# Kernel optimization log

Measured on AMD Instinct MI355X. Metric: run time of the kernel, lower is better.

The kernel has to match this reference:

```python
import jax, jax.numpy as jnp
import numpy as np

N, E = 25000, 400000
HID, EDGE_F, DIM, HEADS, ADY = 128, 16, 3, 8, 64
INNER = int(1.25 * HID)          # 160
MSG_F = 2 * HID + EDGE_F + 1     # 273 (e3, relaxed=False -> 1 distance feature)


def silu(x):
    return x * jax.nn.sigmoid(x)


def ada_ln(x, y, W, b):
    # LayerNorm (no affine) + FiLM conditioning from y
    mu = jnp.mean(x, axis=-1, keepdims=True)
    var = jnp.var(x, axis=-1, keepdims=True)
    xn = (x - mu) * jax.lax.rsqrt(var + 1e-5)
    scale, shift = jnp.split(y @ W + b, 2, axis=-1)
    return xn * (1.0 + scale) + shift


def setup_inputs() -> dict:
    key = jax.random.key(0)
    ks = jax.random.split(key, 32)
    rn = lambda k, shp, s=0.05: (jax.random.normal(k, shp, jnp.float32) * s)
    inp = {
        'h': jax.random.normal(ks[0], (N, HID), jnp.float32),
        'coords': jax.random.normal(ks[1], (N, DIM), jnp.float32),
        'a': jax.random.normal(ks[2], (E, EDGE_F), jnp.float32),
        'y': jax.random.normal(ks[3], (N, ADY), jnp.float32),
        'res': jnp.zeros((N, HID), jnp.float32),
        'src': jax.random.randint(ks[4], (E,), 0, N, jnp.int32),
        'dst': jax.random.randint(ks[5], (E,), 0, N, jnp.int32),
        # edge MLP
        'We1': rn(ks[6], (MSG_F, INNER)), 'be1': jnp.zeros((INNER,), jnp.float32),
        'We2': rn(ks[7], (INNER, INNER)), 'be2': jnp.zeros((INNER,), jnp.float32),
        # coord head (xavier gain 0.001 -> tiny init)
        'Wc': rn(ks[8], (INNER, 1), 0.001),
        # attention/value/output heads
        'Wv': rn(ks[9], (INNER, HID)),
        'Wa': rn(ks[10], (INNER, HEADS)),
        'Wo': rn(ks[11], (HID, HID)),
        # node MLP
        'Wn1': rn(ks[12], (HID, INNER)), 'bn1': jnp.zeros((INNER,), jnp.float32),
        'Wn2': rn(ks[13], (INNER, HID)), 'bn2': jnp.zeros((HID,), jnp.float32),
        # adaptive LayerNorms (FiLM from y)
        'Wf1': rn(ks[14], (ADY, 2 * HID)), 'bf1': jnp.zeros((2 * HID,), jnp.float32),
        'Wf2': rn(ks[15], (ADY, 2 * HID)), 'bf2': jnp.zeros((2 * HID,), jnp.float32),
    }
    return inp


def reference(h, coords, a, y, res, src, dst,
              We1, be1, We2, be2, Wc, Wv, Wa, Wo,
              Wn1, bn1, Wn2, bn2, Wf1, bf1, Wf2, bf2):
    n = h.shape[0]
    heads = Wa.shape[1]
    # --- distance features (e3, relaxed=False): radial only ---
    xs, xd = coords[src], coords[dst]          # [E, 3]
    diffs = xs - xd
    radials = jnp.sum(diffs * diffs, axis=-1, keepdims=True)  # [E, 1]
    # --- edge MLP on gathered features ---
    f = jnp.concatenate([h[src], h[dst], radials, a], axis=-1)  # [E, 273]
    m = silu(f @ We1 + be1)
    m = silu(m @ We2 + be2)                    # [E, inner]
    # --- coordinate messages + scatter-sum to dst ---
    msg_x = (m @ Wc) * diffs / (jnp.sqrt(radials + 1e-5) + 1.0)  # [E, 3]
    coords_out = coords + jax.ops.segment_sum(msg_x, dst, num_segments=n)
    # --- edge softmax over incoming edges per dst node ---
    logits = m @ Wa                             # [E, heads]
    mx = jax.ops.segment_max(logits, dst, num_segments=n)
    ex = jnp.exp(logits - mx[dst])
    den = jax.ops.segment_sum(ex, dst, num_segments=n)
    w = ex / den[dst]                           # [E, heads]
    # --- weighted value aggregation ---
    vals = (m @ Wv).reshape(-1, heads, HID // heads) * w[:, :, None]
    h_agg = jax.ops.segment_sum(vals, dst, num_segments=n).reshape(n, HID)
    f2 = h_agg @ Wo
    res1 = res + f2
    h1 = ada_ln(h + f2, y, Wf1, bf1)
    f3 = silu(h1 @ Wn1 + bn1) @ Wn2 + bn2
    res2 = res1 + f3
    h2 = ada_ln(h1 + f3, y, Wf2, bf2)
    return (h2, coords_out, res2)
```

## Files before the change

kernel.cpp:

```cpp
#include <hip/hip_runtime.h>
#include <math.h>

#define N_NODES 25000
#define N_EDGES 400000
#define HID 128
#define EDGE_F 16
#define ADY 64
#define INNER 160
#define MSG_F 273
#define HEADS 8

#define OUT_CRD (N_NODES * HID)
#define OUT_RES (N_NODES * (HID + 3))

#define FLAG_OFF 0
#define DEN_OFF  256
#define CACC_OFF 800256
#define HAGG_OFF 1100256
#define CNT_OFF  13900256
#define CUR_OFF  14000256
#define PERM_OFF 14100256
#define MEMSET_BYTES 14000256
#define HBF_OFF  15700256
#define YBF_OFF  22100256
#define BIAS_OFF 25300256
#define BW_OFF   25302560

#define WSLICE 3072
#define SM_OFF 512
#define SCR_STRIDE 146

typedef unsigned short u16;
typedef unsigned int u32;
typedef unsigned long long u64;
typedef __attribute__((ext_vector_type(8))) short short8;
typedef __attribute__((ext_vector_type(4))) float f32x4;

__device__ __forceinline__ float bf2f(u16 v) {
    union { u32 u; float f; } x; x.u = ((u32)v) << 16; return x.f;
}
__device__ __forceinline__ u16 f2bf(float f) {
    union { float ff; u32 u; } x; x.ff = f;
    u32 u = x.u;
    u32 rounding = 0x7FFFu + ((u >> 16) & 1u);
    u += rounding;
    return (u16)(u >> 16);
}
__device__ __forceinline__ u32 cvt_pk(float lo, float hi) {
    u32 r;
    asm("v_cvt_pk_bf16_f32 %0, %1, %2" : "=v"(r) : "v"(lo), "v"(hi));
    return r;
}
__device__ __forceinline__ float silu(float z) {
    z = fminf(fmaxf(z, -30000.f), 30000.f);
    return z / (1.0f + __expf(-z));
}

template<bool F32> __device__ __forceinline__ float ldg1(const void* p, size_t i) {
    if (F32) return ((const float*)p)[i];
    return bf2f(((const u16*)p)[i]);
}
template<bool F32> __device__ __forceinline__ void stg1(void* p, size_t i, float v) {
    if (F32) ((float*)p)[i] = v;
    else     ((u16*)p)[i] = f2bf(v);
}
__device__ __forceinline__ float ldany(const void* p, size_t i, bool f32) {
    return f32 ? ((const float*)p)[i] : bf2f(((const u16*)p)[i]);
}
__device__ __forceinline__ void wave_lds_fence() {
    __builtin_amdgcn_wave_barrier();
    __builtin_amdgcn_s_waitcnt(0xc07f);
    __builtin_amdgcn_wave_barrier();
}

__device__ __forceinline__ int a_addr(int k, int lr) {
    return ((k >> 5) << 9) + (((((k & 31) >> 3) << 4) | lr) << 3) + (k & 7);
}

struct CvtArgs {
    const void* src[8];
    u64 dstoff[8];
    int n[8];
};
struct BwArgs {
    const void* We1; const void* We2; const void* Wv; const void* Wa;
    const void* Wc;  const void* Wo;  const void* Wn1; const void* Wn2;
    const void* Wf1; const void* Wf2;
    u64 b1, b2, b3, b4, b5, b6, b7, b8;
};

__global__ __launch_bounds__(256)
void preproc_kernel(const void* hsrc, int* flag, char* ws, CvtArgs args, BwArgs bwa,
                    const int* __restrict__ dstp, int* __restrict__ cnt)
{
    __shared__ float red[256];
    __shared__ int sflag;
    const int t = threadIdx.x;
    {
        const u16* p = (const u16*)hsrc;
        float mx = 0.f;
        for (int i = 0; i < 8; i++) {
            int idx = (t * 8 + i) * 97;
            float v = fabsf(bf2f(p[idx * 2]));
            mx = fmaxf(mx, v);
        }
        red[t] = mx;
        __syncthreads();
        for (int s = 128; s > 0; s >>= 1) {
            if (t < s) red[t] = fmaxf(red[t], red[t + s]);
            __syncthreads();
        }
        if (t == 0) {
            sflag = (red[0] > 1e10f || red[0] == 0.f) ? 1 : 0;
            if (blockIdx.x == 0) flag[0] = sflag;
        }
        __syncthreads();
    }
    const bool f32 = (sflag != 0);
    const int g = blockIdx.x * 256 + t;
    const int stride = gridDim.x * 256;

    for (int i = g; i < N_EDGES; i += stride)
        atomicAdd(&cnt[dstp[i]], 1);

    for (int ten = 0; ten < 8; ten++) {
        const void* s = args.src[ten];
        u16* d = (u16*)(ws + args.dstoff[ten]);
        const int n = args.n[ten];
        if (f32) {
            const float* sf = (const float*)s;
            for (int i = g; i < n; i += stride) d[i] = f2bf(sf[i]);
        } else {
            const u16* su = (const u16*)s;
            for (int i = g; i < n; i += stride) d[i] = su[i];
        }
    }

    u16* b1 = (u16*)(ws + bwa.b1);
    u16* b2 = (u16*)(ws + bwa.b2);
    u16* b3 = (u16*)(ws + bwa.b3);
    u16* b4 = (u16*)(ws + bwa.b4);
    u16* b5 = (u16*)(ws + bwa.b5);
    u16* b6 = (u16*)(ws + bwa.b6);
    u16* b7 = (u16*)(ws + bwa.b7);
    u16* b8 = (u16*)(ws + bwa.b8);
    for (int i = g; i < 5*2*10*512; i += stride) {
        int tt = i >> 9, r = i & 511, l = r >> 3, j = r & 7;
        int c = tt / 20, ks = (tt / 10) % 2, nt = tt % 10;
        int k = c*64 + ks*32 + (l >> 4)*8 + j;
        int n = nt*16 + (l & 15);
        float v = 0.f;
        if (k < MSG_F)      v = ldany(bwa.We1, (size_t)k*INNER + n, f32);
        else if (k == 273)  v = ldany(bwa.We1, (size_t)256*INNER + n, f32);
        b1[i] = f2bf(v);
    }
    for (int i = g; i < 5*10*512; i += stride) {
        int tt = i >> 9, r = i & 511, l = r >> 3, j = r & 7;
        int k5 = tt / 10, nt = tt % 10;
        int k = k5*32 + (l >> 4)*8 + j;
        int n = nt*16 + (l & 15);
        b2[i] = f2bf(ldany(bwa.We2, (size_t)k*INNER + n, f32));
    }
    for (int i = g; i < 5*9*512; i += stride) {
        int tt = i >> 9, r = i & 511, l = r >> 3, j = r & 7;
        int k5 = tt / 9, nt = tt % 9;
        int k = k5*32 + (l >> 4)*8 + j;
        int n = nt*16 + (l & 15);
        float v = 0.f;
        if (n < 128)       v = ldany(bwa.Wv, (size_t)k*HID + n, f32);
        else if (n < 136)  v = ldany(bwa.Wa, (size_t)k*HEADS + (n-128), f32);
        else if (n == 136) v = ldany(bwa.Wc, (size_t)k, f32);
        b3[i] = f2bf(v);
    }
    for (int i = g; i < 4*8*512; i += stride) {
        int tt = i >> 9, r = i & 511, l = r >> 3, j = r & 7;
        int cks = tt / 8, nt = tt % 8;
        int k = cks*32 + (l >> 4)*8 + j;
        int n = nt*16 + (l & 15);
        b4[i] = f2bf(ldany(bwa.Wo, (size_t)k*HID + n, f32));
    }
    for (int i = g; i < 4*10*512; i += stride) {
        int tt = i >> 9, r = i & 511, l = r >> 3, j = r & 7;
        int cks = tt / 10, nt = tt % 10;
        int k = cks*32 + (l >> 4)*8 + j;
        int n = nt*16 + (l & 15);
        b5[i] = f2bf(ldany(bwa.Wn1, (size_t)k*INNER + n, f32));
    }
    for (int i = g; i < 5*8*512; i += stride) {
        int tt = i >> 9, r = i & 511, l = r >> 3, j = r & 7;
        int k5 = tt / 8, nt = tt % 8;
        int k = k5*32 + (l >> 4)*8 + j;
        int n = nt*16 + (l & 15);
        b6[i] = f2bf(ldany(bwa.Wn2, (size_t)k*HID + n, f32));
    }
    for (int i = g; i < 2*16*512; i += stride) {
        int tt = i >> 9, r = i & 511, l = r >> 3, j = r & 7;
        int ks = tt / 16, nt = tt % 16;
        int k = ks*32 + (l >> 4)*8 + j;
        int n = nt*16 + (l & 15);
        b7[i] = f2bf(ldany(bwa.Wf1, (size_t)k*256 + n, f32));
        b8[i] = f2bf(ldany(bwa.Wf2, (size_t)k*256 + n, f32));
    }
}

__global__ __launch_bounds__(1024)
void scan_kernel(const int* __restrict__ cnt, int* __restrict__ cursor)
{
    __shared__ int ssum[1024];
    const int t = threadIdx.x;
    const int base = t * 25;
    int loc[25];
    int s = 0;
    #pragma unroll
    for (int j = 0; j < 25; j++) {
        int i = base + j;
        int v = (i < N_NODES) ? cnt[i] : 0;
        loc[j] = s; s += v;
    }
    ssum[t] = s;
    __syncthreads();
    for (int off = 1; off < 1024; off <<= 1) {
        int v = (t >= off) ? ssum[t - off] : 0;
        __syncthreads();
        ssum[t] += v;
        __syncthreads();
    }
    int offs = (t > 0) ? ssum[t - 1] : 0;
    #pragma unroll
    for (int j = 0; j < 25; j++) {
        int i = base + j;
        if (i < N_NODES) cursor[i] = offs + loc[j];
    }
}

__global__ __launch_bounds__(256)
void scatter_kernel(const int* __restrict__ dstp, int* __restrict__ cursor,
                    int* __restrict__ perm)
{
    int i = blockIdx.x * 256 + threadIdx.x;
    if (i < N_EDGES) {
        int pos = atomicAdd(&cursor[dstp[i]], 1);
        perm[pos] = i;
    }
}

template<bool F32>
__device__ __forceinline__ void edge_body(
    const u16* __restrict__ hbf, const void* coords, const void* a,
    const int* __restrict__ src, const int* __restrict__ dst,
    const int* __restrict__ perm,
    const u16* __restrict__ We1P, const u16* __restrict__ We2P,
    const u16* __restrict__ W3P,
    const u16* __restrict__ cbe1, const u16* __restrict__ cbe2,
    float* __restrict__ den, float* __restrict__ hagg, float* __restrict__ cacc,
    u16* sPool)
{
    const int t   = threadIdx.x;
    const int w   = t >> 6;
    const int l   = t & 63;
    const int col = l & 15;
    const int q   = l >> 4;
    const int e0  = blockIdx.x * 64;
    const int l8  = l << 3;

    u16* sW = sPool + w * WSLICE;

    const int ge2 = perm[e0 + w*16 + col];
    const int s2 = src[ge2];
    const int d2 = dst[ge2];

    short8 afr[8];
    {
        const u16* hs = hbf + (size_t)s2*HID + q*8;
        const u16* hd = hbf + (size_t)d2*HID + q*8;
        #pragma unroll
        for (int kk = 0; kk < 4; kk++) {
            afr[kk]     = *(const short8*)(hs + (kk << 5));
            afr[4 + kk] = *(const short8*)(hd + (kk << 5));
        }
    }

    const int er = l >> 2;
    const int p  = l & 3;
    const int ge = perm[e0 + w*16 + er];
    float dx = 0.f, dy = 0.f, dz = 0.f, invf = 0.f, r2 = 0.f;
    if (p < 2) {
        int s_ = src[ge], d_ = dst[ge];
        dx = ldg1<F32>(coords, (size_t)s_*3+0) - ldg1<F32>(coords, (size_t)d_*3+0);
        dy = ldg1<F32>(coords, (size_t)s_*3+1) - ldg1<F32>(coords, (size_t)d_*3+1);
        dz = ldg1<F32>(coords, (size_t)s_*3+2) - ldg1<F32>(coords, (size_t)d_*3+2);
        r2 = dx*dx + dy*dy + dz*dz;
        invf = 1.0f / (sqrtf(r2 + 1e-5f) + 1.0f);
        __align__(16) u16 tmp[16];
        #pragma unroll
        for (int j = 0; j < 16; j++) tmp[j] = 0;
        if (p == 0) {
            tmp[0] = f2bf(r2);
            for (int j = 0; j < 15; j++)
                tmp[1+j] = f2bf(ldg1<F32>(a, (size_t)ge*EDGE_F + j));
        } else {
            tmp[0] = f2bf(ldg1<F32>(a, (size_t)ge*EDGE_F + 15));
            tmp[1] = f2bf(r2 - bf2f(f2bf(r2)));
        }
        *(uint4*)(sW + (32*p + er)*8)      = ((uint4*)tmp)[0];
        *(uint4*)(sW + (32*p + 16 + er)*8) = ((uint4*)tmp)[1];
    }
    wave_lds_fence();

    f32x4 acc1[10];
    #pragma unroll
    for (int nt = 0; nt < 10; nt++) {
        float v = bf2f(cbe1[nt*16 + col]);
        acc1[nt] = (f32x4){v, v, v, v};
    }
    #pragma unroll
    for (int kk = 0; kk < 8; kk++) {
        const u16* B1 = We1P + ((kk*10) << 9) + l8;
        #pragma unroll
        for (int nt = 0; nt < 10; nt++) {
            short8 b = *(const short8*)(B1 + (nt << 9));
            acc1[nt] = __builtin_amdgcn_mfma_f32_16x16x32_bf16(afr[kk], b, acc1[nt], 0, 0, 0);
        }
    }
    {
        short8 af = *(const short8*)(sW + l8);
        const u16* B1 = We1P + ((8*10) << 9) + l8;
        #pragma unroll
        for (int nt = 0; nt < 10; nt++) {
            short8 b = *(const short8*)(B1 + (nt << 9));
            acc1[nt] = __builtin_amdgcn_mfma_f32_16x16x32_bf16(af, b, acc1[nt], 0, 0, 0);
        }
    }
    const bool lo = (col & 1) == 0;
    const int cb16 = col & ~1;
    #pragma unroll
    for (int nt = 0; nt < 10; nt++) {
        float m0 = silu(acc1[nt][0]);
        float m1 = silu(acc1[nt][1]);
        float m2 = silu(acc1[nt][2]);
        float m3 = silu(acc1[nt][3]);
        float p0 = __shfl_xor(m0, 1);
        float p1 = __shfl_xor(m1, 1);
        float p2 = __shfl_xor(m2, 1);
        float p3 = __shfl_xor(m3, 1);
        int k0 = nt*16 + cb16;
        if (lo) {
            *(u32*)(sW + SM_OFF + a_addr(k0, q*4+0)) = cvt_pk(m0, p0);
            *(u32*)(sW + SM_OFF + a_addr(k0, q*4+1)) = cvt_pk(m1, p1);
        } else {
            *(u32*)(sW + SM_OFF + a_addr(k0, q*4+2)) = cvt_pk(p2, m2);
            *(u32*)(sW + SM_OFF + a_addr(k0, q*4+3)) = cvt_pk(p3, m3);
        }
    }
    wave_lds_fence();

    f32x4 acc2[10];
    #pragma unroll
    for (int nt = 0; nt < 10; nt++) {
        float v = bf2f(cbe2[nt*16 + col]);
        acc2[nt] = (f32x4){v, v, v, v};
    }
    #pragma unroll
    for (int k5 = 0; k5 < 5; k5++) {
        short8 af = *(const short8*)(sW + SM_OFF + (k5 << 9) + l8);
        const u16* B2 = We2P + ((k5*10) << 9) + l8;
        #pragma unroll
        for (int nt = 0; nt < 10; nt++) {
            short8 b = *(const short8*)(B2 + (nt << 9));
            acc2[nt] = __builtin_amdgcn_mfma_f32_16x16x32_bf16(af, b, acc2[nt], 0, 0, 0);
        }
    }
    wave_lds_fence();
    #pragma unroll
    for (int nt = 0; nt < 10; nt++) {
        float m0 = silu(acc2[nt][0]);
        float m1 = silu(acc2[nt][1]);
        float m2 = silu(acc2[nt][2]);
        float m3 = silu(acc2[nt][3]);
        float p0 = __shfl_xor(m0, 1);
        float p1 = __shfl_xor(m1, 1);
        float p2 = __shfl_xor(m2, 1);
        float p3 = __shfl_xor(m3, 1);
        int k0 = nt*16 + cb16;
        if (lo) {
            *(u32*)(sW + SM_OFF + a_addr(k0, q*4+0)) = cvt_pk(m0, p0);
            *(u32*)(sW + SM_OFF + a_addr(k0, q*4+1)) = cvt_pk(m1, p1);
        } else {
            *(u32*)(sW + SM_OFF + a_addr(k0, q*4+2)) = cvt_pk(p2, m2);
            *(u32*)(sW + SM_OFF + a_addr(k0, q*4+3)) = cvt_pk(p3, m3);
        }
    }
    wave_lds_fence();

    f32x4 acc3[9];
    #pragma unroll
    for (int nt = 0; nt < 9; nt++) acc3[nt] = (f32x4){0.f, 0.f, 0.f, 0.f};
    #pragma unroll
    for (int k5 = 0; k5 < 5; k5++) {
        short8 af = *(const short8*)(sW + SM_OFF + (k5 << 9) + l8);
        const u16* B3 = W3P + ((k5*9) << 9) + l8;
        #pragma unroll
        for (int nt = 0; nt < 9; nt++) {
            short8 b = *(const short8*)(B3 + (nt << 9));
            acc3[nt] = __builtin_amdgcn_mfma_f32_16x16x32_bf16(af, b, acc3[nt], 0, 0, 0);
        }
    }
    wave_lds_fence();

    int dsts[16];
    #pragma unroll
    for (int row = 0; row < 16; row++) dsts[row] = __shfl(d2, row);
    float dxv[4], dyv[4], dzv[4], ivv[4];
    #pragma unroll
    for (int rr = 0; rr < 4; rr++) {
        int sl = (q*4 + rr) << 2;
        dxv[rr] = __shfl(dx, sl); dyv[rr] = __shfl(dy, sl);
        dzv[rr] = __shfl(dz, sl); ivv[rr] = __shfl(invf, sl);
    }

    {
        float exv[4] = {0.f, 0.f, 0.f, 0.f};
        if (col < 8) {
            #pragma unroll
            for (int rr = 0; rr < 4; rr++)
                exv[rr] = __expf(fminf(fmaxf(acc3[8][rr], -30.f), 30.f));
        }
        #pragma unroll
        for (int nt = 0; nt < 8; nt++) {
            float ex0 = __shfl(exv[0], q*16 + nt);
            float ex1 = __shfl(exv[1], q*16 + nt);
            float ex2 = __shfl(exv[2], q*16 + nt);
            float ex3 = __shfl(exv[3], q*16 + nt);
            float v0 = acc3[nt][0] * ex0;
            float v1 = acc3[nt][1] * ex1;
            float v2 = acc3[nt][2] * ex2;
            float v3 = acc3[nt][3] * ex3;
            float p0 = __shfl_xor(v0, 1);
            float p1 = __shfl_xor(v1, 1);
            float p2 = __shfl_xor(v2, 1);
            float p3 = __shfl_xor(v3, 1);
            int cb = nt*16 + cb16;
            int rowA = q*4 + (lo ? 0 : 2);
            u32 wA = lo ? cvt_pk(v0, p0) : cvt_pk(p2, v2);
            u32 wB = lo ? cvt_pk(v1, p1) : cvt_pk(p3, v3);
            *(u32*)(&sW[rowA*SCR_STRIDE + cb])       = wA;
            *(u32*)(&sW[(rowA+1)*SCR_STRIDE + cb])   = wB;
        }
        if (col < 8) {
            #pragma unroll
            for (int rr = 0; rr < 4; rr++)
                sW[(q*4 + rr)*SCR_STRIDE + 128 + col] = f2bf(exv[rr]);
        }
        if (col == 8) {
            #pragma unroll
            for (int rr = 0; rr < 4; rr++) {
                float lc = fminf(fmaxf(acc3[8][rr], -1e6f), 1e6f) * ivv[rr];
                sW[(q*4 + rr)*SCR_STRIDE + 136] = f2bf(lc * dxv[rr]);
                sW[(q*4 + rr)*SCR_STRIDE + 137] = f2bf(lc * dyv[rr]);
                sW[(q*4 + rr)*SCR_STRIDE + 138] = f2bf(lc * dzv[rr]);
            }
        }
    }
    wave_lds_fence();

    #pragma unroll
    for (int pass = 0; pass < 3; pass++) {
        int c = pass*64 + l;
        bool act = c < 139;
        float accu = 0.f;
        int prevd = dsts[0];
        #pragma unroll
        for (int row = 0; row < 16; row++) {
            int d = dsts[row];
            if (d != prevd) {
                if (act) {
                    if (c < 128)      atomicAdd(&hagg[(size_t)prevd*HID + c], accu);
                    else if (c < 136) atomicAdd(&den[(size_t)prevd*8 + (c-128)], accu);
                    else              atomicAdd(&cacc[(size_t)prevd*3 + (c-136)], accu);
                }
                accu = 0.f; prevd = d;
            }
            if (act) accu += bf2f(sW[row*SCR_STRIDE + c]);
        }
        if (act) {
            if (c < 128)      atomicAdd(&hagg[(size_t)prevd*HID + c], accu);
            else if (c < 136) atomicAdd(&den[(size_t)prevd*8 + (c-128)], accu);
            else              atomicAdd(&cacc[(size_t)prevd*3 + (c-136)], accu);
        }
    }
}

__global__ __launch_bounds__(256, 4)
void edge_kernel(const int* __restrict__ flag,
                 const u16* __restrict__ hbf, const void* coords, const void* a,
                 const int* __restrict__ src, const int* __restrict__ dst,
                 const int* __restrict__ perm,
                 const u16* __restrict__ We1P, const u16* __restrict__ We2P,
                 const u16* __restrict__ W3P,
                 const u16* __restrict__ cbe1, const u16* __restrict__ cbe2,
                 float* __restrict__ den, float* __restrict__ hagg,
                 float* __restrict__ cacc)
{
    __shared__ __align__(16) u16 sPool[4 * WSLICE];
    if (*flag)
        edge_body<true>(hbf, coords, a, src, dst, perm, We1P, We2P, W3P,
                        cbe1, cbe2, den, hagg, cacc, sPool);
    else
        edge_body<false>(hbf, coords, a, src, dst, perm, We1P, We2P, W3P,
                         cbe1, cbe2, den, hagg, cacc, sPool);
}

template<bool F32>
__device__ __forceinline__ void node_body(
    const u16* __restrict__ hbf, const void* res, const void* coords,
    const u16* __restrict__ ybf,
    const float* __restrict__ den, const float* __restrict__ hagg,
    const float* __restrict__ cacc,
    const u16* __restrict__ WoP, const u16* __restrict__ Wn1P,
    const u16* __restrict__ Wn2P, const u16* __restrict__ Wf1P,
    const u16* __restrict__ Wf2P,
    const u16* __restrict__ cbn1, const u16* __restrict__ cbn2,
    const u16* __restrict__ cbf1, const u16* __restrict__ cbf2,
    void* out, u16* sScr)
{
    const int t = threadIdx.x;
    const int w = t >> 6, l = t & 63, col = l & 15, q = l >> 4;
    const int nodew = blockIdx.x * 64 + w * 16;
    const int mynode = nodew + col;
    const bool okA = mynode < N_NODES;
    const int l8 = l << 3;
    const bool lo = (col & 1) == 0;
    const int cb16 = col & ~1;
    u16* sc = sScr + w * 16 * 168;

    int gm[4]; bool okC[4];
    #pragma unroll
    for (int r = 0; r < 4; r++) { gm[r] = nodew + q*4 + r; okC[r] = gm[r] < N_NODES; }

    f32x4 aF2[8];
    #pragma unroll
    for (int nt = 0; nt < 8; nt++) aF2[nt] = (f32x4){0.f,0.f,0.f,0.f};
    #pragma unroll
    for (int c = 0; c < 2; c++) {
        #pragma unroll
        for (int ks = 0; ks < 2; ks++) {
            const int kbase = c*64 + ks*32 + q*8;
            union { u32 w[4]; short8 v; } u;
            if (okA) {
                float dd = den[(size_t)mynode*8 + (kbase >> 4)];
                float inv = dd > 0.f ? 1.f/dd : 0.f;
                const float4* gp = (const float4*)(hagg + (size_t)mynode*HID + kbase);
                float4 v0 = gp[0], v1 = gp[1];
                u.w[0] = cvt_pk(v0.x*inv, v0.y*inv);
                u.w[1] = cvt_pk(v0.z*inv, v0.w*inv);
                u.w[2] = cvt_pk(v1.x*inv, v1.y*inv);
                u.w[3] = cvt_pk(v1.z*inv, v1.w*inv);
            } else {
                #pragma unroll
                for (int j = 0; j < 4; j++) u.w[j] = 0;
            }
            const u16* B = WoP + (((c*2 + ks)*8) << 9) + l8;
            #pragma unroll
            for (int nt = 0; nt < 8; nt++) {
                short8 b = *(const short8*)(B + (nt << 9));
                aF2[nt] = __builtin_amdgcn_mfma_f32_16x16x32_bf16(u.v, b, aF2[nt], 0, 0, 0);
            }
        }
    }

    f32x4 aFl[16];
    #pragma unroll
    for (int nt = 0; nt < 16; nt++) {
        float v = bf2f(cbf1[nt*16 + col]);
        aFl[nt] = (f32x4){v,v,v,v};
    }
    #pragma unroll
    for (int ks = 0; ks < 2; ks++) {
        short8 af;
        if (okA) af = *(const short8*)(ybf + (size_t)mynode*ADY + ks*32 + q*8);
        else { union { u16 s[8]; short8 v; } z; for (int j=0;j<8;j++) z.s[j]=0; af = z.v; }
        const u16* B = Wf1P + ((ks*16) << 9) + l8;
        #pragma unroll
        for (int nt = 0; nt < 16; nt++) {
            short8 b = *(const short8*)(B + (nt << 9));
            aFl[nt] = __builtin_amdgcn_mfma_f32_16x16x32_bf16(af, b, aFl[nt], 0, 0, 0);
        }
    }

    float h1c[8][4], r1c[8][4];
    {
        float xv[8][4], s[4], ss[4];
        #pragma unroll
        for (int r = 0; r < 4; r++) { s[r] = 0.f; ss[r] = 0.f; }
        #pragma unroll
        for (int nt = 0; nt < 8; nt++)
            #pragma unroll
            for (int r = 0; r < 4; r++) {
                float hv = okC[r] ? bf2f(hbf[(size_t)gm[r]*HID + nt*16 + col]) : 0.f;
                float x = hv + aF2[nt][r];
                xv[nt][r] = x; s[r] += x; ss[r] += x*x;
            }
        #pragma unroll
        for (int r = 0; r < 4; r++)
            for (int off = 1; off <= 8; off <<= 1) {
                s[r]  += __shfl_xor(s[r], off);
                ss[r] += __shfl_xor(ss[r], off);
            }
        #pragma unroll
        for (int r = 0; r < 4; r++) {
            float mu = s[r] * (1.f/128.f);
            float var = ss[r] * (1.f/128.f) - mu*mu;
            float rs = rsqrtf(fmaxf(var, 0.f) + 1e-5f);
            #pragma unroll
            for (int nt = 0; nt < 8; nt++) {
                float h1 = (xv[nt][r]-mu)*rs*(1.f+aFl[nt][r]) + aFl[nt+8][r];
                h1c[nt][r] = h1;
                float rv = okC[r] ? ldg1<F32>(res, (size_t)gm[r]*HID + nt*16 + col) : 0.f;
                r1c[nt][r] = rv + aF2[nt][r];
            }
        }
        #pragma unroll
        for (int nt = 0; nt < 8; nt++) {
            float p0 = __shfl_xor(h1c[nt][0], 1);
            float p1 = __shfl_xor(h1c[nt][1], 1);
            float p2 = __shfl_xor(h1c[nt][2], 1);
            float p3 = __shfl_xor(h1c[nt][3], 1);
            int cb = nt*16 + cb16;
            if (lo) {
                *(u32*)(&sc[(q*4 + 0)*168 + cb]) = cvt_pk(h1c[nt][0], p0);
                *(u32*)(&sc[(q*4 + 1)*168 + cb]) = cvt_pk(h1c[nt][1], p1);
            } else {
                *(u32*)(&sc[(q*4 + 2)*168 + cb]) = cvt_pk(p2, h1c[nt][2]);
                *(u32*)(&sc[(q*4 + 3)*168 + cb]) = cvt_pk(p3, h1c[nt][3]);
            }
        }
    }
    wave_lds_fence();

    f32x4 aT[10];
    #pragma unroll
    for (int nt = 0; nt < 10; nt++) {
        float v = bf2f(cbn1[nt*16 + col]);
        aT[nt] = (f32x4){v,v,v,v};
    }
    #pragma unroll
    for (int c = 0; c < 2; c++) {
        #pragma unroll
        for (int ks = 0; ks < 2; ks++) {
            short8 af = *(const short8*)(sc + col*168 + c*64 + ks*32 + q*8);
            const u16* B = Wn1P + (((c*2 + ks)*10) << 9) + l8;
            #pragma unroll
            for (int nt = 0; nt < 10; nt++) {
                short8 b = *(const short8*)(B + (nt << 9));
                aT[nt] = __builtin_amdgcn_mfma_f32_16x16x32_bf16(af, b, aT[nt], 0, 0, 0);
            }
        }
    }
    wave_lds_fence();
    #pragma unroll
    for (int nt = 0; nt < 10; nt++) {
        float m0 = silu(aT[nt][0]);
        float m1 = silu(aT[nt][1]);
        float m2 = silu(aT[nt][2]);
        float m3 = silu(aT[nt][3]);
        float p0 = __shfl_xor(m0, 1);
        float p1 = __shfl_xor(m1, 1);
        float p2 = __shfl_xor(m2, 1);
        float p3 = __shfl_xor(m3, 1);
        int cb = nt*16 + cb16;
        if (lo) {
            *(u32*)(&sc[(q*4 + 0)*168 + cb]) = cvt_pk(m0, p0);
            *(u32*)(&sc[(q*4 + 1)*168 + cb]) = cvt_pk(m1, p1);
        } else {
            *(u32*)(&sc[(q*4 + 2)*168 + cb]) = cvt_pk(p2, m2);
            *(u32*)(&sc[(q*4 + 3)*168 + cb]) = cvt_pk(p3, m3);
        }
    }
    wave_lds_fence();

    f32x4 aF3[8];
    #pragma unroll
    for (int nt = 0; nt < 8; nt++) {
        float v = bf2f(cbn2[nt*16 + col]);
        aF3[nt] = (f32x4){v,v,v,v};
    }
    #pragma unroll
    for (int k5 = 0; k5 < 5; k5++) {
        short8 af = *(const short8*)(sc + col*168 + k5*32 + q*8);
        const u16* B = Wn2P + ((k5*8) << 9) + l8;
        #pragma unroll
        for (int nt = 0; nt < 8; nt++) {
            short8 b = *(const short8*)(B + (nt << 9));
            aF3[nt] = __builtin_amdgcn_mfma_f32_16x16x32_bf16(af, b, aF3[nt], 0, 0, 0);
        }
    }

    #pragma unroll
    for (int nt = 0; nt < 16; nt++) {
        float v = bf2f(cbf2[nt*16 + col]);
        aFl[nt] = (f32x4){v,v,v,v};
    }
    #pragma unroll
    for (int ks = 0; ks < 2; ks++) {
        short8 af;
        if (okA) af = *(const short8*)(ybf + (size_t)mynode*ADY + ks*32 + q*8);
        else { union { u16 s[8]; short8 v; } z; for (int j=0;j<8;j++) z.s[j]=0; af = z.v; }
        const u16* B = Wf2P + ((ks*16) << 9) + l8;
        #pragma unroll
        for (int nt = 0; nt < 16; nt++) {
            short8 b = *(const short8*)(B + (nt << 9));
            aFl[nt] = __builtin_amdgcn_mfma_f32_16x16x32_bf16(af, b, aFl[nt], 0, 0, 0);
        }
    }

    {
        float xv[8][4], s[4], ss[4];
        #pragma unroll
        for (int r = 0; r < 4; r++) { s[r] = 0.f; ss[r] = 0.f; }
        #pragma unroll
        for (int nt = 0; nt < 8; nt++)
            #pragma unroll
            for (int r = 0; r < 4; r++) {
                float x = h1c[nt][r] + aF3[nt][r];
                xv[nt][r] = x; s[r] += x; ss[r] += x*x;
            }
        #pragma unroll
        for (int r = 0; r < 4; r++)
            for (int off = 1; off <= 8; off <<= 1) {
                s[r]  += __shfl_xor(s[r], off);
                ss[r] += __shfl_xor(ss[r], off);
            }
        #pragma unroll
        for (int r = 0; r < 4; r++) {
            float mu = s[r] * (1.f/128.f);
            float var = ss[r] * (1.f/128.f) - mu*mu;
            float rs = rsqrtf(fmaxf(var, 0.f) + 1e-5f);
            if (okC[r]) {
                #pragma unroll
                for (int nt = 0; nt < 8; nt++) {
                    int n = nt*16 + col;
                    float h2 = (xv[nt][r]-mu)*rs*(1.f+aFl[nt][r]) + aFl[nt+8][r];
                    stg1<F32>(out, (size_t)gm[r]*HID + n, h2);
                    stg1<F32>(out, (size_t)OUT_RES + (size_t)gm[r]*HID + n,
                              r1c[nt][r] + aF3[nt][r]);
                }
            }
        }
    }

    if (q == 0 && okA) {
        #pragma unroll
        for (int j = 0; j < 3; j++)
            stg1<F32>(out, (size_t)OUT_CRD + (size_t)mynode*3 + j,
                      ldg1<F32>(coords, (size_t)mynode*3 + j) + cacc[(size_t)mynode*3 + j]);
    }
}

__global__ __launch_bounds__(256, 2)
void node_kernel(const int* __restrict__ flag,
                 const u16* __restrict__ hbf, const void* res, const void* coords,
                 const u16* __restrict__ ybf,
                 const float* __restrict__ den, const float* __restrict__ hagg,
                 const float* __restrict__ cacc,
                 const u16* __restrict__ WoP, const u16* __restrict__ Wn1P,
                 const u16* __restrict__ Wn2P, const u16* __restrict__ Wf1P,
                 const u16* __restrict__ Wf2P,
                 const u16* __restrict__ cbn1, const u16* __restrict__ cbn2,
                 const u16* __restrict__ cbf1, const u16* __restrict__ cbf2,
                 void* out)
{
    __shared__ __align__(16) u16 sScr[4 * 16 * 168];
    if (*flag)
        node_body<true>(hbf, res, coords, ybf, den, hagg, cacc, WoP, Wn1P, Wn2P,
                        Wf1P, Wf2P, cbn1, cbn2, cbf1, cbf2, out, sScr);
    else
        node_body<false>(hbf, res, coords, ybf, den, hagg, cacc, WoP, Wn1P, Wn2P,
                         Wf1P, Wf2P, cbn1, cbn2, cbf1, cbf2, out, sScr);
}

extern "C" void kernel_launch(void* const* d_in, const int* in_sizes, int n_in,
                              void* d_out, int out_size, void* d_ws, size_t ws_size,
                              hipStream_t stream)
{
    const void* h      = d_in[0];
    const void* coords = d_in[1];
    const void* a      = d_in[2];
    const void* y      = d_in[3];
    const void* res    = d_in[4];
    const int* src     = (const int*)d_in[5];
    const int* dst     = (const int*)d_in[6];

    char* ws = (char*)d_ws;
    int*   flag   = (int*)(ws + FLAG_OFF);
    float* den    = (float*)(ws + DEN_OFF);
    float* cacc   = (float*)(ws + CACC_OFF);
    float* hagg   = (float*)(ws + HAGG_OFF);
    int*   cnt    = (int*)(ws + CNT_OFF);
    int*   cursor = (int*)(ws + CUR_OFF);
    int*   perm   = (int*)(ws + PERM_OFF);
    u16*   hbf    = (u16*)(ws + HBF_OFF);
    u16*   ybf    = (u16*)(ws + YBF_OFF);

    CvtArgs args;
    const int cvtn[8]   = {160, 160, 160, 128, 256, 256, N_NODES*HID, N_NODES*ADY};
    const int cvtsrc[8] = {8, 10, 16, 18, 20, 22, 0, 3};
    u64 boff[8];
    u64 bo = BIAS_OFF;
    for (int i = 0; i < 6; i++) {
        boff[i] = bo;
        bo += ((u64)cvtn[i] * 2 + 15) & ~(u64)15;
    }
    boff[6] = HBF_OFF;
    boff[7] = YBF_OFF;
    for (int i = 0; i < 8; i++) {
        args.src[i] = d_in[cvtsrc[i]];
        args.dstoff[i] = boff[i];
        args.n[i] = cvtn[i];
    }
    const u16* cbe1 = (const u16*)(ws + boff[0]);
    const u16* cbe2 = (const u16*)(ws + boff[1]);
    const u16* cbn1 = (const u16*)(ws + boff[2]);
    const u16* cbn2 = (const u16*)(ws + boff[3]);
    const u16* cbf1 = (const u16*)(ws + boff[4]);
    const u16* cbf2 = (const u16*)(ws + boff[5]);

    BwArgs bwa;
    bwa.We1 = d_in[7];  bwa.We2 = d_in[9];  bwa.Wv = d_in[12]; bwa.Wa = d_in[13];
    bwa.Wc  = d_in[11]; bwa.Wo  = d_in[14]; bwa.Wn1 = d_in[15]; bwa.Wn2 = d_in[17];
    bwa.Wf1 = d_in[19]; bwa.Wf2 = d_in[21];
    bwa.b1 = BW_OFF;
    bwa.b2 = bwa.b1 + (u64)5*2*10*512*2;
    bwa.b3 = bwa.b2 + (u64)5*10*512*2;
    bwa.b4 = bwa.b3 + (u64)5*9*512*2;
    bwa.b5 = bwa.b4 + (u64)4*8*512*2;
    bwa.b6 = bwa.b5 + (u64)4*10*512*2;
    bwa.b7 = bwa.b6 + (u64)5*8*512*2;
    bwa.b8 = bwa.b7 + (u64)2*16*512*2;
    const u16* We1P = (const u16*)(ws + bwa.b1);
    const u16* We2P = (const u16*)(ws + bwa.b2);
    const u16* W3P  = (const u16*)(ws + bwa.b3);
    const u16* WoP  = (const u16*)(ws + bwa.b4);
    const u16* Wn1P = (const u16*)(ws + bwa.b5);
    const u16* Wn2P = (const u16*)(ws + bwa.b6);
    const u16* Wf1P = (const u16*)(ws + bwa.b7);
    const u16* Wf2P = (const u16*)(ws + bwa.b8);

    hipMemsetAsync(d_ws, 0, MEMSET_BYTES, stream);

    preproc_kernel<<<256, 256, 0, stream>>>(h, flag, ws, args, bwa, dst, cnt);

    scan_kernel<<<1, 1024, 0, stream>>>(cnt, cursor);

    scatter_kernel<<<(N_EDGES + 255)/256, 256, 0, stream>>>(dst, cursor, perm);

    edge_kernel<<<N_EDGES/64, 256, 0, stream>>>(flag, hbf, coords, a, src, dst, perm,
                                                We1P, We2P, W3P, cbe1, cbe2,
                                                den, hagg, cacc);

    node_kernel<<<(N_NODES + 63)/64, 256, 0, stream>>>(
        flag, hbf, res, coords, ybf, den, hagg, cacc,
        WoP, Wn1P, Wn2P, Wf1P, Wf2P, cbn1, cbn2, cbf1, cbf2, d_out);
}
```

Measured before the change: 493.4 us.

## Fuse CSR scan and scatter into preproc kernel using software grid barriers

The separate scan and scatter kernels are merged into the preprocessing kernel. A spin-wait grid barrier on an atomic counter separates the phases, and the single-block scan becomes a two-level block-parallel scan, removing two kernel launches and their serialization gaps. The edge kernel also moves the h-row gathers after the coordinate/LDS setup, likely to shorten register live ranges or reorder memory latency. The grid barrier assumes all 256 blocks are co-resident, which holds on this GPU but is not guaranteed in general. The barrier counter lives inside the region the existing memset zeroes, so it is reset on every call.

```diff
diff --git a/kernel.cpp b/kernel.cpp
--- a/kernel.cpp
+++ b/kernel.cpp
@@ -14,17 +14,20 @@
 #define OUT_RES (N_NODES * (HID + 3))
 
 #define FLAG_OFF 0
+#define BAR_OFF  16
 #define DEN_OFF  256
 #define CACC_OFF 800256
 #define HAGG_OFF 1100256
 #define CNT_OFF  13900256
 #define CUR_OFF  14000256
+#define MEMSET_BYTES 14000256
 #define PERM_OFF 14100256
-#define MEMSET_BYTES 14000256
-#define HBF_OFF  15700256
-#define YBF_OFF  22100256
-#define BIAS_OFF 25300256
-#define BW_OFF   25302560
+#define BSUM_OFF 15700256
+#define BBASE_OFF 15701280
+#define HBF_OFF  15702304
+#define YBF_OFF  22102304
+#define BIAS_OFF 25302304
+#define BW_OFF   25304608
 
 #define WSLICE 3072
 #define SM_OFF 512
@@ -75,6 +78,17 @@
 
 __device__ __forceinline__ int a_addr(int k, int lr) {
     return ((k >> 5) << 9) + (((((k & 31) >> 3) << 4) | lr) << 3) + (k & 7);
+}
+
+__device__ __forceinline__ void grid_bar(int* bar, int target) {
+    __threadfence();
+    __syncthreads();
+    if (threadIdx.x == 0) {
+        __hip_atomic_fetch_add(bar, 1, __ATOMIC_ACQ_REL, __HIP_MEMORY_SCOPE_AGENT);
+        while (__hip_atomic_load(bar, __ATOMIC_ACQUIRE, __HIP_MEMORY_SCOPE_AGENT) < target)
+            __builtin_amdgcn_s_sleep(8);
+    }
+    __syncthreads();
 }
 
 struct CvtArgs {
@@ -91,11 +105,17 @@
 
 __global__ __launch_bounds__(256)
 void preproc_kernel(const void* hsrc, int* flag, char* ws, CvtArgs args, BwArgs bwa,
-                    const int* __restrict__ dstp, int* __restrict__ cnt)
+                    const int* __restrict__ dstp, int* __restrict__ cnt,
+                    int* __restrict__ cursor, int* __restrict__ perm,
+                    int* __restrict__ bar, int* __restrict__ bsum,
+                    int* __restrict__ bbase)
 {
     __shared__ float red[256];
     __shared__ int sflag;
+    __shared__ int sscan[128];
+    __shared__ int s2a[256];
     const int t = threadIdx.x;
+    const int b = blockIdx.x;
     {
         const u16* p = (const u16*)hsrc;
         float mx = 0.f;
@@ -112,12 +132,12 @@
         }
         if (t == 0) {
             sflag = (red[0] > 1e10f || red[0] == 0.f) ? 1 : 0;
-            if (blockIdx.x == 0) flag[0] = sflag;
+            if (b == 0) flag[0] = sflag;
         }
         __syncthreads();
     }
     const bool f32 = (sflag != 0);
-    const int g = blockIdx.x * 256 + t;
+    const int g = b * 256 + t;
     const int stride = gridDim.x * 256;
 
     for (int i = g; i < N_EDGES; i += stride)
@@ -201,44 +221,55 @@
         b7[i] = f2bf(ldany(bwa.Wf1, (size_t)k*256 + n, f32));
         b8[i] = f2bf(ldany(bwa.Wf2, (size_t)k*256 + n, f32));
     }
-}
-
-__global__ __launch_bounds__(1024)
-void scan_kernel(const int* __restrict__ cnt, int* __restrict__ cursor)
-{
-    __shared__ int ssum[1024];
-    const int t = threadIdx.x;
-    const int base = t * 25;
-    int loc[25];
-    int s = 0;
-    #pragma unroll
-    for (int j = 0; j < 25; j++) {
-        int i = base + j;
-        int v = (i < N_NODES) ? cnt[i] : 0;
-        loc[j] = s; s += v;
-    }
-    ssum[t] = s;
-    __syncthreads();
-    for (int off = 1; off < 1024; off <<= 1) {
-        int v = (t >= off) ? ssum[t - off] : 0;
+
+    grid_bar(bar, 256);
+
+    int myv = 0;
+    if (b < 250) {
+        if (t < 128) {
+            int bin = b*100 + t;
+            myv = (t < 100)
+                ? __hip_atomic_load(&cnt[bin], __ATOMIC_RELAXED, __HIP_MEMORY_SCOPE_AGENT)
+                : 0;
+            sscan[t] = myv;
+        }
         __syncthreads();
-        ssum[t] += v;
+        for (int off = 1; off < 128; off <<= 1) {
+            int x = (t < 128 && t >= off) ? sscan[t - off] : 0;
+            __syncthreads();
+            if (t < 128) sscan[t] += x;
+            __syncthreads();
+        }
+        if (t == 127)
+            __hip_atomic_store(&bsum[b], sscan[127], __ATOMIC_RELEASE, __HIP_MEMORY_SCOPE_AGENT);
+    } else {
+        if (t == 0)
+            __hip_atomic_store(&bsum[b], 0, __ATOMIC_RELEASE, __HIP_MEMORY_SCOPE_AGENT);
+    }
+    grid_bar(bar, 512);
+
+    if (b == 0) {
+        int v2 = __hip_atomic_load(&bsum[t], __ATOMIC_RELAXED, __HIP_MEMORY_SCOPE_AGENT);
+        s2a[t] = v2;
         __syncthreads();
-    }
-    int offs = (t > 0) ? ssum[t - 1] : 0;
-    #pragma unroll
-    for (int j = 0; j < 25; j++) {
-        int i = base + j;
-        if (i < N_NODES) cursor[i] = offs + loc[j];
-    }
-}
-
-__global__ __launch_bounds__(256)
-void scatter_kernel(const int* __restrict__ dstp, int* __restrict__ cursor,
-                    int* __restrict__ perm)
-{
-    int i = blockIdx.x * 256 + threadIdx.x;
-    if (i < N_EDGES) {
+        for (int off = 1; off < 256; off <<= 1) {
+            int x = (t >= off) ? s2a[t - off] : 0;
+            __syncthreads();
+            s2a[t] += x;
+            __syncthreads();
+        }
+        __hip_atomic_store(&bbase[t], s2a[t] - v2, __ATOMIC_RELEASE, __HIP_MEMORY_SCOPE_AGENT);
+    }
+    grid_bar(bar, 768);
+
+    if (b < 250 && t < 100) {
+        int base = __hip_atomic_load(&bbase[b], __ATOMIC_RELAXED, __HIP_MEMORY_SCOPE_AGENT);
+        __hip_atomic_store(&cursor[b*100 + t], base + sscan[t] - myv,
+                           __ATOMIC_RELEASE, __HIP_MEMORY_SCOPE_AGENT);
+    }
+    grid_bar(bar, 1024);
+
+    for (int i = g; i < N_EDGES; i += stride) {
         int pos = atomicAdd(&cursor[dstp[i]], 1);
         perm[pos] = i;
     }
@@ -269,17 +300,6 @@
     const int s2 = src[ge2];
     const int d2 = dst[ge2];
 
-    short8 afr[8];
-    {
-        const u16* hs = hbf + (size_t)s2*HID + q*8;
-        const u16* hd = hbf + (size_t)d2*HID + q*8;
-        #pragma unroll
-        for (int kk = 0; kk < 4; kk++) {
-            afr[kk]     = *(const short8*)(hs + (kk << 5));
-            afr[4 + kk] = *(const short8*)(hd + (kk << 5));
-        }
-    }
-
     const int er = l >> 2;
     const int p  = l & 3;
     const int ge = perm[e0 + w*16 + er];
@@ -304,6 +324,17 @@
         }
         *(uint4*)(sW + (32*p + er)*8)      = ((uint4*)tmp)[0];
         *(uint4*)(sW + (32*p + 16 + er)*8) = ((uint4*)tmp)[1];
+    }
+
+    short8 afr[8];
+    {
+        const u16* hs = hbf + (size_t)s2*HID + q*8;
+        const u16* hd = hbf + (size_t)d2*HID + q*8;
+        #pragma unroll
+        for (int kk = 0; kk < 4; kk++) {
+            afr[kk]     = *(const short8*)(hs + (kk << 5));
+            afr[4 + kk] = *(const short8*)(hd + (kk << 5));
+        }
     }
     wave_lds_fence();
 
@@ -792,12 +823,15 @@
 
     char* ws = (char*)d_ws;
     int*   flag   = (int*)(ws + FLAG_OFF);
+    int*   bar    = (int*)(ws + BAR_OFF);
     float* den    = (float*)(ws + DEN_OFF);
     float* cacc   = (float*)(ws + CACC_OFF);
     float* hagg   = (float*)(ws + HAGG_OFF);
     int*   cnt    = (int*)(ws + CNT_OFF);
     int*   cursor = (int*)(ws + CUR_OFF);
     int*   perm   = (int*)(ws + PERM_OFF);
+    int*   bsum   = (int*)(ws + BSUM_OFF);
+    int*   bbase  = (int*)(ws + BBASE_OFF);
     u16*   hbf    = (u16*)(ws + HBF_OFF);
     u16*   ybf    = (u16*)(ws + YBF_OFF);
 
@@ -847,11 +881,8 @@
 
     hipMemsetAsync(d_ws, 0, MEMSET_BYTES, stream);
 
-    preproc_kernel<<<256, 256, 0, stream>>>(h, flag, ws, args, bwa, dst, cnt);
-
-    scan_kernel<<<1, 1024, 0, stream>>>(cnt, cursor);
-
-    scatter_kernel<<<(N_EDGES + 255)/256, 256, 0, stream>>>(dst, cursor, perm);
+    preproc_kernel<<<256, 256, 0, stream>>>(h, flag, ws, args, bwa, dst, cnt,
+                                            cursor, perm, bar, bsum, bbase);
 
     edge_kernel<<<N_EDGES/64, 256, 0, stream>>>(flag, hbf, coords, a, src, dst, perm,
                                                 We1P, We2P, W3P, cbe1, cbe2,
```

Measured after the change: 618.5 us. 1.25x slower.
